# Kernel optimization log

Measured on AMD Instinct MI355X. Metric: run time of the kernel, lower is better.

## Reference

```python
import jax, jax.numpy as jnp
from jax import lax
import numpy as np

B, T, F = 4096, 512, 63
NOINPUTS, HIDDEN, OUT = 64, 1024, 1  # NOINPUTS = F + OUT


def setup_inputs() -> dict:
    key = jax.random.key(0)
    k1, k2, k3, k4, k5, k6 = jax.random.split(key, 6)
    inputs = jax.random.normal(k1, (B, T, F), dtype=jnp.float32)
    labels = jax.random.normal(k2, (B, T, 1), dtype=jnp.float32)
    # FFNN params: Linear(noinputs, hidden) -> ReLU -> Linear(hidden, out)
    s1 = 1.0 / np.sqrt(NOINPUTS)
    s2 = 1.0 / np.sqrt(HIDDEN)
    W1 = jax.random.uniform(k3, (NOINPUTS, HIDDEN), jnp.float32, -s1, s1)
    b1 = jax.random.uniform(k4, (HIDDEN,), jnp.float32, -s1, s1)
    W2 = jax.random.uniform(k5, (HIDDEN, OUT), jnp.float32, -s2, s2)
    b2 = jax.random.uniform(k6, (OUT,), jnp.float32, -s2, s2)
    return {"inputs": inputs, "labels": labels, "W1": W1, "b1": b1, "W2": W2, "b2": b2}


def reference(inputs, labels, W1, b1, W2, b2):
    # output_size == 1 branch: result tensor starts as zeros (B,1,1);
    # each step feeds [inputs[:,t,:], last_pred] through the MLP.
    Bb = inputs.shape[0]

    def step(prev_pred, x_t):  # prev_pred: (B,1), x_t: (B,F)
        mi = jnp.concatenate([x_t, prev_pred], axis=1)      # (B, noinputs)
        h = jax.nn.relu(mi @ W1 + b1)                        # (B, hidden)
        pred = h @ W2 + b2                                   # (B, 1)
        return pred, pred

    xs = jnp.swapaxes(inputs[:, 1:, :], 0, 1)                # (T-1, B, F)
    init = jnp.zeros((Bb, 1), inputs.dtype)
    _, preds = lax.scan(step, init, xs)                      # (T-1, B, 1)
    preds = jnp.swapaxes(preds, 0, 1)                        # (B, T-1, 1)
    zero0 = jnp.zeros((Bb, 1, 1), inputs.dtype)
    return jnp.concatenate([zero0, preds], axis=1)           # (B, T, 1)
```

## Files before the change

kernel.cpp:

```cpp
#include <hip/hip_runtime.h>


#define TT 512
#define FF 63
#define HID 1024

typedef __attribute__((ext_vector_type(8))) short short8;
typedef __attribute__((ext_vector_type(4))) float f32x4;
typedef __attribute__((ext_vector_type(4))) int i32x4;
typedef __attribute__((ext_vector_type(8))) _Float16 h16x8;

__device__ __forceinline__ unsigned short f2bf(float f) {
  union { float f; unsigned u; } v; v.f = f;
  unsigned r = v.u + 0x7FFFu + ((v.u >> 16) & 1u);
  return (unsigned short)(r >> 16);
}

__device__ __forceinline__ void lds_barrier() {
  asm volatile("s_waitcnt lgkmcnt(0)" ::: "memory");
  __builtin_amdgcn_s_barrier();
  asm volatile("" ::: "memory");
}

__device__ __forceinline__ int pkh(float a, float b) {
  auto h = __builtin_amdgcn_cvt_pkrtz(fmaxf(a, 0.f), fmaxf(b, 0.f));
  return __builtin_bit_cast(int, h);
}

__global__ __launch_bounds__(512, 2)
void ffnn_ar_kernel(const float* __restrict__ x,
                    const float* __restrict__ W1,
                    const float* __restrict__ b1,
                    const float* __restrict__ W2,
                    const float* __restrict__ b2p,
                    float* __restrict__ out) {
  __shared__ __align__(16) unsigned short lds_A[2][16][72];
  __shared__ __align__(16) float lds_part[2][8][16];

  const int tid  = threadIdx.x;
  const int lane = tid & 63;
  const int w    = tid >> 6;
  const int c    = lane & 15;
  const int g    = lane >> 4;
  const int br   = blockIdx.x * 16;

  short8 bfr[8][2];
#pragma unroll
  for (int i = 0; i < 8; ++i) {
    const int n = (w * 8 + i) * 16 + c;
#pragma unroll
    for (int ks = 0; ks < 2; ++ks) {
      short8 f;
#pragma unroll
      for (int j = 0; j < 8; ++j) f[j] = (short)f2bf(W1[(ks * 32 + g * 8 + j) * HID + n]);
      bfr[i][ks] = f;
    }
  }
  f32x4 b1v[8];
#pragma unroll
  for (int i = 0; i < 8; ++i) {
    const int nb = (w * 8 + i) * 16 + g * 4;
    b1v[i] = (f32x4){b1[nb], b1[nb + 1], b1[nb + 2], b1[nb + 3]};
  }
  h16x8 a2f[4];
#pragma unroll
  for (int i2 = 0; i2 < 4; ++i2) {
    h16x8 f;
#pragma unroll
    for (int j = 0; j < 8; ++j)
      f[j] = (_Float16)W2[(w * 8 + 2 * i2 + (j >> 2)) * 16 + g * 4 + (j & 3)];
    a2f[i2] = f;
  }
  const float b2 = b2p[0];
  const float b2w = (w == 0) ? b2 : 0.f;

  const int srow = tid >> 5;
  const int sl   = tid & 31;
  const long rowbase = (long)(br + srow) * (TT * FF);

  lds_A[1][srow][sl] = f2bf(x[rowbase + FF + sl]);
  if (sl < 31) lds_A[1][srow][32 + sl] = f2bf(x[rowbase + FF + 32 + sl]);
  if (tid < 128) reinterpret_cast<float*>(lds_part)[tid] = 0.f;
  if (tid < 16) out[(long)(br + tid) * TT] = 0.f;

  float s0a = x[rowbase + 2 * FF + sl];
  float s0b = (sl < 31) ? x[rowbase + 2 * FF + 32 + sl] : 0.f;
  float s1a = x[rowbase + 3 * FF + sl];
  float s1b = (sl < 31) ? x[rowbase + 3 * FF + 32 + sl] : 0.f;

  lds_barrier();

#define STEP(T, CUR, SA, SB)                                                        \
  {                                                                                 \
    \
    const float* pp = &lds_part[(CUR) ^ 1][0][c];                                   \
    const float pc = ((pp[0] + pp[16]) + (pp[32] + pp[48])) +                       \
                     ((pp[64] + pp[80]) + (pp[96] + pp[112]));                      \
    if (w == 0 && g == 0) out[(long)(br + c) * TT + ((T) - 1)] = pc;                \
                    \
    const short8 xb0 = *reinterpret_cast<const short8*>(&lds_A[CUR][c][g * 8]);     \
    short8 xb1 = *reinterpret_cast<const short8*>(&lds_A[CUR][c][32 + g * 8]);      \
    if (g == 3) xb1[7] = (short)f2bf(pc);                                           \
        \
    f32x4 acc[8];                                                                   \
    _Pragma("unroll") for (int i = 0; i < 8; ++i) {                                 \
      f32x4 z4 = __builtin_amdgcn_mfma_f32_16x16x32_bf16(bfr[i][0], xb0, b1v[i], 0, 0, 0); \
      acc[i] = __builtin_amdgcn_mfma_f32_16x16x32_bf16(bfr[i][1], xb1, z4, 0, 0, 0);\
    }                                                                               \
          \
    lds_A[(CUR) ^ 1][srow][sl] = f2bf(SA);                                          \
    if (sl < 31) lds_A[(CUR) ^ 1][srow][32 + sl] = f2bf(SB);                        \
    {                                                                               \
      const int tp = ((T) + 3 < TT) ? (T) + 3 : TT - 1;                             \
      SA = x[rowbase + (long)tp * FF + sl];                                         \
      if (sl < 31) SB = x[rowbase + (long)tp * FF + 32 + sl];                       \
    }                                                                               \
    \
    f32x4 p2a = {b2w, b2w, b2w, b2w};                                               \
    f32x4 p2b = {0.f, 0.f, 0.f, 0.f};                                               \
    _Pragma("unroll") for (int i2 = 0; i2 < 4; ++i2) {                              \
      const f32x4 u = acc[2 * i2], v = acc[2 * i2 + 1];                             \
      const h16x8 hf = __builtin_bit_cast(h16x8, (i32x4){                           \
          pkh(u[0], u[1]), pkh(u[2], u[3]), pkh(v[0], v[1]), pkh(v[2], v[3])});     \
      if (i2 & 1)                                                                   \
        p2b = __builtin_amdgcn_mfma_f32_16x16x32_f16(a2f[i2], hf, p2b, 0, 0, 0);    \
      else                                                                          \
        p2a = __builtin_amdgcn_mfma_f32_16x16x32_f16(a2f[i2], hf, p2a, 0, 0, 0);    \
    }                                                                               \
                              \
    if (g == 0) lds_part[CUR][w][c] = p2a[0] + p2b[0];                              \
    lds_barrier();                                                                  \
  }

#pragma unroll 1
  for (int t = 1; t + 1 < TT; t += 2) {
    STEP(t, 1, s0a, s0b)
    STEP(t + 1, 0, s1a, s1b)
  }
  STEP(TT - 1, 1, s0a, s0b)

  {
    const float* pp = &lds_part[1][0][c];
    const float pc = ((pp[0] + pp[16]) + (pp[32] + pp[48])) +
                     ((pp[64] + pp[80]) + (pp[96] + pp[112]));
    if (w == 0 && g == 0) out[(long)(br + c) * TT + (TT - 1)] = pc;
  }
#undef STEP
}

extern "C" void kernel_launch(void* const* d_in, const int* in_sizes, int n_in,
                              void* d_out, int out_size, void* d_ws, size_t ws_size,
                              hipStream_t stream) {
  const float* x   = (const float*)d_in[0];
  const float* W1  = (const float*)d_in[2];
  const float* b1  = (const float*)d_in[3];
  const float* W2  = (const float*)d_in[4];
  const float* b2  = (const float*)d_in[5];
  float* out = (float*)d_out;

  ffnn_ar_kernel<<<256, 512, 0, stream>>>(x, W1, b1, W2, b2, out);
}
```

Before: 389.7 us.

## Take prev-pred feedback out of the MFMA as an fp32 rank-1 update

The previous prediction is no longer packed into the last element of the MFMA B operand. Instead it is added after the first-layer MFMAs as pc*W1[63] with fmaf, using preloaded per-lane W1 row-63 values. This lets the first-layer MFMAs start without waiting on the cross-wave reduction of the previous prediction, shortening the serial per-timestep critical path. The change also switches the first layer from bf16 to f16 operands and transposes the partial-sum LDS buffer so the reduction reads two float4 vectors. It adds a few VALU FMAs per step and relies on f16 range being enough for the inputs.

```diff
diff --git a/kernel.cpp b/kernel.cpp
--- a/kernel.cpp
+++ b/kernel.cpp
@@ -5,16 +5,9 @@
 #define FF 63
 #define HID 1024
 
-typedef __attribute__((ext_vector_type(8))) short short8;
 typedef __attribute__((ext_vector_type(4))) float f32x4;
 typedef __attribute__((ext_vector_type(4))) int i32x4;
 typedef __attribute__((ext_vector_type(8))) _Float16 h16x8;
-
-__device__ __forceinline__ unsigned short f2bf(float f) {
-  union { float f; unsigned u; } v; v.f = f;
-  unsigned r = v.u + 0x7FFFu + ((v.u >> 16) & 1u);
-  return (unsigned short)(r >> 16);
-}
 
 __device__ __forceinline__ void lds_barrier() {
   asm volatile("s_waitcnt lgkmcnt(0)" ::: "memory");
@@ -34,8 +27,8 @@
                     const float* __restrict__ W2,
                     const float* __restrict__ b2p,
                     float* __restrict__ out) {
-  __shared__ __align__(16) unsigned short lds_A[2][16][72];
-  __shared__ __align__(16) float lds_part[2][8][16];
+  __shared__ __align__(16) _Float16 lds_A[2][16][72];
+  __shared__ __align__(16) float lds_part[2][16][12];
 
   const int tid  = threadIdx.x;
   const int lane = tid & 63;
@@ -44,23 +37,25 @@
   const int g    = lane >> 4;
   const int br   = blockIdx.x * 16;
 
-  short8 bfr[8][2];
+  h16x8 bfr[8][2];
 #pragma unroll
   for (int i = 0; i < 8; ++i) {
     const int n = (w * 8 + i) * 16 + c;
 #pragma unroll
     for (int ks = 0; ks < 2; ++ks) {
-      short8 f;
+      h16x8 f;
 #pragma unroll
-      for (int j = 0; j < 8; ++j) f[j] = (short)f2bf(W1[(ks * 32 + g * 8 + j) * HID + n]);
+      for (int j = 0; j < 8; ++j) f[j] = (_Float16)W1[(ks * 32 + g * 8 + j) * HID + n];
       bfr[i][ks] = f;
     }
   }
-  f32x4 b1v[8];
+  f32x4 b1v[8], w63v[8];
 #pragma unroll
   for (int i = 0; i < 8; ++i) {
     const int nb = (w * 8 + i) * 16 + g * 4;
-    b1v[i] = (f32x4){b1[nb], b1[nb + 1], b1[nb + 2], b1[nb + 3]};
+    b1v[i]  = (f32x4){b1[nb], b1[nb + 1], b1[nb + 2], b1[nb + 3]};
+    w63v[i] = (f32x4){W1[63 * HID + nb], W1[63 * HID + nb + 1],
+                      W1[63 * HID + nb + 2], W1[63 * HID + nb + 3]};
   }
   h16x8 a2f[4];
 #pragma unroll
@@ -78,9 +73,10 @@
   const int sl   = tid & 31;
   const long rowbase = (long)(br + srow) * (TT * FF);
 
-  lds_A[1][srow][sl] = f2bf(x[rowbase + FF + sl]);
-  if (sl < 31) lds_A[1][srow][32 + sl] = f2bf(x[rowbase + FF + 32 + sl]);
-  if (tid < 128) reinterpret_cast<float*>(lds_part)[tid] = 0.f;
+  lds_A[1][srow][sl] = (_Float16)x[rowbase + FF + sl];
+  if (sl < 31) lds_A[1][srow][32 + sl] = (_Float16)x[rowbase + FF + 32 + sl];
+  if (tid < 16) { lds_A[0][tid][63] = (_Float16)0.f; lds_A[1][tid][63] = (_Float16)0.f; }
+  if (tid < 384) reinterpret_cast<float*>(lds_part)[tid] = 0.f;
   if (tid < 16) out[(long)(br + tid) * TT] = 0.f;
 
   float s0a = x[rowbase + 2 * FF + sl];
@@ -92,24 +88,24 @@
 
 #define STEP(T, CUR, SA, SB)                                                        \
   {                                                                                 \
-    \
-    const float* pp = &lds_part[(CUR) ^ 1][0][c];                                   \
-    const float pc = ((pp[0] + pp[16]) + (pp[32] + pp[48])) +                       \
-                     ((pp[64] + pp[80]) + (pp[96] + pp[112]));                      \
-    if (w == 0 && g == 0) out[(long)(br + c) * TT + ((T) - 1)] = pc;                \
-                    \
-    const short8 xb0 = *reinterpret_cast<const short8*>(&lds_A[CUR][c][g * 8]);     \
-    short8 xb1 = *reinterpret_cast<const short8*>(&lds_A[CUR][c][32 + g * 8]);      \
-    if (g == 3) xb1[7] = (short)f2bf(pc);                                           \
+               \
+    const h16x8 xb0 = *reinterpret_cast<const h16x8*>(&lds_A[CUR][c][g * 8]);       \
+    const h16x8 xb1 = *reinterpret_cast<const h16x8*>(&lds_A[CUR][c][32 + g * 8]);  \
+      \
+    const f32x4 v0 = *reinterpret_cast<const f32x4*>(&lds_part[(CUR) ^ 1][c][0]);   \
+    const f32x4 v1 = *reinterpret_cast<const f32x4*>(&lds_part[(CUR) ^ 1][c][4]);   \
+    const float pc = ((v0[0] + v0[1]) + (v0[2] + v0[3])) +                          \
+                     ((v1[0] + v1[1]) + (v1[2] + v1[3]));                           \
         \
     f32x4 acc[8];                                                                   \
     _Pragma("unroll") for (int i = 0; i < 8; ++i) {                                 \
-      f32x4 z4 = __builtin_amdgcn_mfma_f32_16x16x32_bf16(bfr[i][0], xb0, b1v[i], 0, 0, 0); \
-      acc[i] = __builtin_amdgcn_mfma_f32_16x16x32_bf16(bfr[i][1], xb1, z4, 0, 0, 0);\
+      f32x4 z4 = __builtin_amdgcn_mfma_f32_16x16x32_f16(bfr[i][0], xb0, b1v[i], 0, 0, 0); \
+      acc[i] = __builtin_amdgcn_mfma_f32_16x16x32_f16(bfr[i][1], xb1, z4, 0, 0, 0); \
     }                                                                               \
+    if (w == 0 && g == 0) out[(long)(br + c) * TT + ((T) - 1)] = pc;                \
           \
-    lds_A[(CUR) ^ 1][srow][sl] = f2bf(SA);                                          \
-    if (sl < 31) lds_A[(CUR) ^ 1][srow][32 + sl] = f2bf(SB);                        \
+    lds_A[(CUR) ^ 1][srow][sl] = (_Float16)SA;                                      \
+    if (sl < 31) lds_A[(CUR) ^ 1][srow][32 + sl] = (_Float16)SB;                    \
     {                                                                               \
       const int tp = ((T) + 3 < TT) ? (T) + 3 : TT - 1;                             \
       SA = x[rowbase + (long)tp * FF + sl];                                         \
@@ -120,15 +116,19 @@
     f32x4 p2b = {0.f, 0.f, 0.f, 0.f};                                               \
     _Pragma("unroll") for (int i2 = 0; i2 < 4; ++i2) {                              \
       const f32x4 u = acc[2 * i2], v = acc[2 * i2 + 1];                             \
+      const f32x4 wu = w63v[2 * i2], wv = w63v[2 * i2 + 1];                         \
       const h16x8 hf = __builtin_bit_cast(h16x8, (i32x4){                           \
-          pkh(u[0], u[1]), pkh(u[2], u[3]), pkh(v[0], v[1]), pkh(v[2], v[3])});     \
+          pkh(fmaf(pc, wu[0], u[0]), fmaf(pc, wu[1], u[1])),                        \
+          pkh(fmaf(pc, wu[2], u[2]), fmaf(pc, wu[3], u[3])),                        \
+          pkh(fmaf(pc, wv[0], v[0]), fmaf(pc, wv[1], v[1])),                        \
+          pkh(fmaf(pc, wv[2], v[2]), fmaf(pc, wv[3], v[3]))});                      \
       if (i2 & 1)                                                                   \
         p2b = __builtin_amdgcn_mfma_f32_16x16x32_f16(a2f[i2], hf, p2b, 0, 0, 0);    \
       else                                                                          \
         p2a = __builtin_amdgcn_mfma_f32_16x16x32_f16(a2f[i2], hf, p2a, 0, 0, 0);    \
     }                                                                               \
-                              \
-    if (g == 0) lds_part[CUR][w][c] = p2a[0] + p2b[0];                              \
+                          \
+    if (g == 0) lds_part[CUR][c][w] = p2a[0] + p2b[0];                              \
     lds_barrier();                                                                  \
   }
 
@@ -140,9 +140,10 @@
   STEP(TT - 1, 1, s0a, s0b)
 
   {
-    const float* pp = &lds_part[1][0][c];
-    const float pc = ((pp[0] + pp[16]) + (pp[32] + pp[48])) +
-                     ((pp[64] + pp[80]) + (pp[96] + pp[112]));
+    const f32x4 v0 = *reinterpret_cast<const f32x4*>(&lds_part[1][c][0]);
+    const f32x4 v1 = *reinterpret_cast<const f32x4*>(&lds_part[1][c][4]);
+    const float pc = ((v0[0] + v0[1]) + (v0[2] + v0[3])) +
+                     ((v1[0] + v1[1]) + (v1[2] + v1[3]));
     if (w == 0 && g == 0) out[(long)(br + c) * TT + (TT - 1)] = pc;
   }
 #undef STEP
```

New measurement: 349.7 us. 1.11x faster.
